# Kernel tuning notes

Hardware: AMD Instinct MI355X
Metric: run time of the kernel (lower is better)

The kernel has to match this reference:

```python
import jax, jax.numpy as jnp
import numpy as np

N = 20000      # nodes
E = 640000     # edges
H = 128        # hidden_channels
NB = 16        # num_angle_bins


def setup_inputs() -> dict:
    key = jax.random.key(0)
    ks = jax.random.split(key, 12)
    s = 0.05
    return {
        "x": jax.random.normal(ks[0], (N, H), jnp.float32),
        "pos": jax.random.normal(ks[1], (N, 3), jnp.float32),
        "edge_index": jax.random.randint(ks[2], (2, E), 0, N, dtype=jnp.int32).astype(jnp.int64),
        # edge_mlp: Linear(2H,H) -> silu -> Linear(H,H); weights stored [in,out]
        "W1": jax.random.normal(ks[3], (2 * H, H), jnp.float32) * s,
        "b1": jnp.zeros((H,), jnp.float32),
        "W2": jax.random.normal(ks[4], (H, H), jnp.float32) * s,
        "b2": jnp.zeros((H,), jnp.float32),
        "Wq": jax.random.normal(ks[5], (H, H), jnp.float32) * s,
        "bq": jnp.zeros((H,), jnp.float32),
        "Wk": jax.random.normal(ks[6], (H, H), jnp.float32) * s,
        "bk": jnp.zeros((H,), jnp.float32),
        "Wv": jax.random.normal(ks[7], (H, H), jnp.float32) * s,
        "bv": jnp.zeros((H,), jnp.float32),
    }


def reference(x, pos, edge_index, W1, b1, W2, b2, Wq, bq, Wk, bk, Wv, bv):
    num_nodes, hidden = x.shape
    num_bins = NB
    src = edge_index[0]  # node_i in torch code; PyG suffix _j gathers with this
    dst = edge_index[1]  # node_j in torch code; PyG suffix _i / aggregation index

    # per-edge embedding from endpoint node features  [E, H]
    h = jnp.concatenate([x[src], x[dst]], axis=-1)
    e = jax.nn.silu(h @ W1 + b1) @ W2 + b2

    # unit edge vectors  [E, 3]
    ev = pos[dst] - pos[src]
    ev = ev / (jnp.linalg.norm(ev, axis=1, keepdims=True) + 1e-8)

    q = e @ Wq + bq
    k = e @ Wk + bk
    v = e @ Wv + bv  # computed in torch forward but unused in message (kept for faithfulness)

    # PyG gathers these per-EDGE tensors by NODE indices (node_dim=0) -- replicate exactly
    e_j = e[src]           # [E, H]
    ev_i = ev[dst]         # [E, 3]
    ev_j = ev[src]         # [E, 3]
    q_i = q[dst]           # [E, H]
    k_j = k[src]           # [E, H]

    cos_theta = jnp.clip(jnp.sum(ev_i * ev_j, axis=-1), -1.0, 1.0)  # [E]
    angle_bins = jnp.linspace(-1.0, 1.0, num_bins + 1)
    bin_ids = jnp.clip(jnp.searchsorted(angle_bins, cos_theta, side="left") - 1, 0, num_bins - 1)

    attn_logits = jnp.sum(q_i * k_j, axis=-1) * (1.0 / np.sqrt(hidden))  # [E]

    # grouped softmax over (target_node, angle_bin) pairs, then weighted scatter-add
    group = dst * num_bins + bin_ids                     # [E]
    num_seg = num_nodes * num_bins
    m = jax.ops.segment_max(attn_logits, group, num_segments=num_seg)
    ex = jnp.exp(attn_logits - m[group])
    den = jax.ops.segment_sum(ex, group, num_segments=num_seg)
    attn = ex / (den[group] + 1e-16)                     # [E]

    summed = jax.ops.segment_sum(e_j * attn[:, None], group, num_segments=num_seg)  # [N*B, H]
    out = summed.reshape(num_nodes, num_bins, hidden)
    out = jnp.transpose(out, (0, 2, 1)).reshape(num_nodes, hidden * num_bins)  # [N, H*B]
    return out
```

## Files before the change

### kernel.cpp

```cpp
#include <hip/hip_runtime.h>

#define NN 20000
#define NE 640000
#define HH 128
#define NBIN 16
#define RSQRT_H 0.08838834764831845f

typedef short bf16x8 __attribute__((ext_vector_type(8)));
typedef float f32x4 __attribute__((ext_vector_type(4)));

__device__ __forceinline__ float b2f(unsigned short u) {
    return __uint_as_float(((unsigned)u) << 16);
}
__device__ __forceinline__ unsigned short f2b(float f) {
    unsigned u = __float_as_uint(f);
    unsigned r = (u + 0x7fffu + ((u >> 16) & 1u)) >> 16;
    return (unsigned short)r;
}
__device__ __forceinline__ int clampn(int v) {
    return min(max(v, 0), NN - 1);
}
__device__ __forceinline__ float dotdw(unsigned a, unsigned b) {
    float lo = __uint_as_float(a << 16) * __uint_as_float(b << 16);
    float hi = __uint_as_float(a & 0xffff0000u) * __uint_as_float(b & 0xffff0000u);
    return lo + hi;
}

__global__ void k_prep_w(const float* __restrict__ W1, const float* __restrict__ W2,
                         const float* __restrict__ Wq, const float* __restrict__ Wk,
                         ushort* __restrict__ W1T, ushort* __restrict__ W2T,
                         ushort* __restrict__ WqkT) {
    int i = blockIdx.x * 256 + threadIdx.x;
    if (i < 128 * 256) {
        int c = i >> 8, k = i & 255;
        W1T[i] = f2b(W1[k * 128 + c]);
    }
    if (i < 128 * 128) {
        int c = i >> 7, k = i & 127;
        W2T[i] = f2b(W2[k * 128 + c]);
    }
    if (i < 256 * 128) {
        int c = i >> 7, k = i & 127;
        float v = (c < 128) ? Wq[k * 128 + c] * RSQRT_H : Wk[k * 128 + (c - 128)];
        WqkT[i] = f2b(v);
    }
}

__global__ void k_prep_x(const float* __restrict__ x, ushort* __restrict__ xb) {
    int i = blockIdx.x * 256 + threadIdx.x;
    if (i >= NN * HH / 4) return;
    float4 v = ((const float4*)x)[i];
    ushort4 o;
    o.x = f2b(v.x); o.y = f2b(v.y); o.z = f2b(v.z); o.w = f2b(v.w);
    ((ushort4*)xb)[i] = o;
}

__global__ void k_ev(const int* __restrict__ ei, const float* __restrict__ pos,
                     float4* __restrict__ ev4) {
    int n = blockIdx.x * 256 + threadIdx.x;
    if (n >= NN) return;
    int s = clampn(ei[n]), d = clampn(ei[NE + n]);
    float dx = __fsub_rn(pos[d * 3 + 0], pos[s * 3 + 0]);
    float dy = __fsub_rn(pos[d * 3 + 1], pos[s * 3 + 1]);
    float dz = __fsub_rn(pos[d * 3 + 2], pos[s * 3 + 2]);
    float nsq = __fadd_rn(__fadd_rn(__fmul_rn(dx, dx), __fmul_rn(dy, dy)), __fmul_rn(dz, dz));
    float den = __fadd_rn(__fsqrt_rn(nsq), 1e-8f);
    float4 o;
    o.x = __fdiv_rn(dx, den); o.y = __fdiv_rn(dy, den); o.z = __fdiv_rn(dz, den); o.w = 0.f;
    ev4[n] = o;
}

__global__ __launch_bounds__(256) void k_mlp(
    const int* __restrict__ ei, const ushort* __restrict__ xb,
    const ushort* __restrict__ W1T, const ushort* __restrict__ W2T,
    const ushort* __restrict__ WqkT,
    const float* __restrict__ b1, const float* __restrict__ b2,
    const float* __restrict__ bq, const float* __restrict__ bk,
    ushort* __restrict__ ebuf, ushort* __restrict__ qbuf, ushort* __restrict__ kbuf)
{
    __shared__ ushort A[64][264];
    __shared__ ushort T[4][16][136];
    __shared__ ushort Eb[4][16][136];
    __shared__ int SN[64], DN[64];

    const int tid = threadIdx.x;
    const int wave = tid >> 6, lane = tid & 63;
    const int rw = lane & 15, kq = lane >> 4;
    const int m0 = blockIdx.x * 64;

    if (tid < 64)        SN[tid]      = (m0 + tid < NN)      ? clampn(ei[m0 + tid]) : 0;
    else if (tid < 128)  DN[tid - 64] = (m0 + tid - 64 < NN) ? clampn(ei[NE + m0 + tid - 64]) : 0;
    __syncthreads();

    const unsigned* x32 = (const unsigned*)xb;
    #pragma unroll
    for (int it = 0; it < 32; ++it) {
        int flat = tid + 256 * it;
        int r = flat >> 7, w = flat & 127;
        int node = (w < 64) ? SN[r] : DN[r];
        unsigned val = x32[node * 64 + (w & 63)];
        *(unsigned*)&A[r][2 * w] = val;
    }
    __syncthreads();

    f32x4 acc[8];
    #pragma unroll
    for (int c = 0; c < 8; c++) acc[c] = (f32x4){0.f, 0.f, 0.f, 0.f};
    for (int k0 = 0; k0 < 256; k0 += 32) {
        bf16x8 a = *(const bf16x8*)&A[wave * 16 + rw][k0 + 8 * kq];
        #pragma unroll
        for (int c = 0; c < 8; c++) {
            bf16x8 b = *(const bf16x8*)&W1T[(c * 16 + rw) * 256 + k0 + 8 * kq];
            acc[c] = __builtin_amdgcn_mfma_f32_16x16x32_bf16(a, b, acc[c], 0, 0, 0);
        }
    }
    #pragma unroll
    for (int c = 0; c < 8; c++) {
        float bias = b1[c * 16 + rw];
        #pragma unroll
        for (int r = 0; r < 4; r++) {
            float v = acc[c][r] + bias;
            float s = v / (1.f + __expf(-v));
            T[wave][kq * 4 + r][c * 16 + rw] = f2b(s);
        }
    }
    __syncthreads();

    f32x4 acc2[8];
    #pragma unroll
    for (int c = 0; c < 8; c++) acc2[c] = (f32x4){0.f, 0.f, 0.f, 0.f};
    for (int k0 = 0; k0 < 128; k0 += 32) {
        bf16x8 a = *(const bf16x8*)&T[wave][rw][k0 + 8 * kq];
        #pragma unroll
        for (int c = 0; c < 8; c++) {
            bf16x8 b = *(const bf16x8*)&W2T[(c * 16 + rw) * 128 + k0 + 8 * kq];
            acc2[c] = __builtin_amdgcn_mfma_f32_16x16x32_bf16(a, b, acc2[c], 0, 0, 0);
        }
    }
    #pragma unroll
    for (int c = 0; c < 8; c++) {
        float bias = b2[c * 16 + rw];
        #pragma unroll
        for (int r = 0; r < 4; r++) {
            float v = acc2[c][r] + bias;
            ushort hv = f2b(v);
            Eb[wave][kq * 4 + r][c * 16 + rw] = hv;
            int n = m0 + wave * 16 + kq * 4 + r;
            if (n < NN) ebuf[n * HH + c * 16 + rw] = hv;
        }
    }
    __syncthreads();

    f32x4 acc3[16];
    #pragma unroll
    for (int c = 0; c < 16; c++) acc3[c] = (f32x4){0.f, 0.f, 0.f, 0.f};
    for (int k0 = 0; k0 < 128; k0 += 32) {
        bf16x8 a = *(const bf16x8*)&Eb[wave][rw][k0 + 8 * kq];
        #pragma unroll
        for (int c = 0; c < 16; c++) {
            bf16x8 b = *(const bf16x8*)&WqkT[(c * 16 + rw) * 128 + k0 + 8 * kq];
            acc3[c] = __builtin_amdgcn_mfma_f32_16x16x32_bf16(a, b, acc3[c], 0, 0, 0);
        }
    }
    #pragma unroll
    for (int c = 0; c < 16; c++) {
        int col = c * 16 + rw;
        float bias = (col < 128) ? bq[col] * RSQRT_H : bk[col - 128];
        #pragma unroll
        for (int r = 0; r < 4; r++) {
            float v = acc3[c][r] + bias;
            int n = m0 + wave * 16 + kq * 4 + r;
            if (n < NN) {
                if (col < 128) qbuf[n * HH + col] = f2b(v);
                else           kbuf[n * HH + col - 128] = f2b(v);
            }
        }
    }
}

__global__ void k_hist(const int* __restrict__ ei, unsigned* __restrict__ cnt) {
    int e = blockIdx.x * 256 + threadIdx.x;
    if (e < NE) atomicAdd(&cnt[clampn(ei[NE + e])], 1u);
}

__global__ __launch_bounds__(1024) void k_scan(const unsigned* __restrict__ cnt,
                                               unsigned* __restrict__ starts,
                                               unsigned* __restrict__ cursor) {
    __shared__ unsigned vals[20480];
    __shared__ unsigned wsum[16];
    const int t = threadIdx.x;
    #pragma unroll
    for (int i = 0; i < 20; i++) {
        int idx = i * 1024 + t;
        vals[idx] = (idx < NN) ? cnt[idx] : 0u;
    }
    __syncthreads();
    const int base = t * 20;
    unsigned loc[20];
    unsigned s = 0;
    #pragma unroll
    for (int i = 0; i < 20; i++) { loc[i] = s; s += vals[base + i]; }
    const int lane = t & 63, wv = t >> 6;
    unsigned inc = s;
    #pragma unroll
    for (int o = 1; o < 64; o <<= 1) {
        unsigned y = __shfl_up(inc, o);
        if (lane >= o) inc += y;
    }
    if (lane == 63) wsum[wv] = inc;
    __syncthreads();
    unsigned wbase = 0;
    for (int i = 0; i < wv; i++) wbase += wsum[i];
    unsigned excl = wbase + inc - s;
    #pragma unroll
    for (int i = 0; i < 20; i++) {
        int idx = base + i;
        if (idx < NN) {
            unsigned val = excl + loc[i];
            starts[idx] = val;
            cursor[idx] = val;
        }
    }
    if (t == 1023) starts[NN] = wbase + inc;
}

__global__ __launch_bounds__(256) void k_edge(
    const int* __restrict__ ei, const ushort* __restrict__ qbuf,
    const ushort* __restrict__ kbuf, const float4* __restrict__ ev4,
    unsigned* __restrict__ cursor, uint2* __restrict__ sorted)
{
    int tid = blockIdx.x * 256 + threadIdx.x;
    int e = tid >> 2;
    int r = tid & 3;
    if (e >= NE) return;
    int s = clampn(ei[e]), d = clampn(ei[NE + e]);

    const uint4* q4 = (const uint4*)qbuf;
    const uint4* k4 = (const uint4*)kbuf;
    float p = 0.f;
    #pragma unroll
    for (int i = 0; i < 4; i++) {
        uint4 qw = q4[d * 16 + r * 4 + i];
        uint4 kw = k4[s * 16 + r * 4 + i];
        p += dotdw(qw.x, kw.x) + dotdw(qw.y, kw.y) + dotdw(qw.z, kw.z) + dotdw(qw.w, kw.w);
    }
    p += __shfl_xor(p, 1);
    p += __shfl_xor(p, 2);

    if (r == 0) {
        float4 vi = ev4[d], vj = ev4[s];
        float cosv = __fadd_rn(__fadd_rn(__fmul_rn(vi.x, vj.x), __fmul_rn(vi.y, vj.y)),
                               __fmul_rn(vi.z, vj.z));
        cosv = fminf(fmaxf(cosv, -1.f), 1.f);
        int cntb = 0;
        #pragma unroll
        for (int i = 0; i <= 16; i++) cntb += ((-1.f + 0.125f * (float)i) < cosv) ? 1 : 0;
        int b = min(max(cntb - 1, 0), NBIN - 1);
        unsigned pos = atomicAdd(&cursor[d], 1u);
        sorted[pos] = make_uint2(__float_as_uint(p), (unsigned)((s << 4) | b));
    }
}

__global__ __launch_bounds__(256) void k_node(
    const unsigned* __restrict__ starts, const uint2* __restrict__ sorted,
    const ushort* __restrict__ ebuf, float* __restrict__ out)
{
    const int wave = threadIdx.x >> 6, lane = threadIdx.x & 63;
    const int n = blockIdx.x * 4 + wave;
    __shared__ float tile[4][NBIN][132];
    __shared__ float den[4][NBIN];

    float* tw = &tile[wave][0][0];
    #pragma unroll
    for (int i = 0; i < 33; i++) {
        int idx = lane + 64 * i;
        if (idx < NBIN * 132) tw[idx] = 0.f;
    }
    if (lane < NBIN) den[wave][lane] = 0.f;

    const unsigned s0 = starts[n];
    const int deg = (int)(starts[n + 1] - s0);

    for (int j0 = 0; j0 < deg; j0 += 64) {
        int j = j0 + lane;
        if (j < deg) {
            uint2 m = sorted[s0 + j];
            atomicAdd(&den[wave][m.y & 15u], __expf(__uint_as_float(m.x)));
        }
    }
    if (lane < NBIN) den[wave][lane] = 1.f / (den[wave][lane] + 1e-16f);

    const unsigned* erow = (const unsigned*)ebuf;
    uint2 mN[4];
    #pragma unroll
    for (int i = 0; i < 4; i++)
        mN[i] = (i < deg) ? sorted[s0 + i] : make_uint2(0u, 0u);
    for (int jb = 0; jb < deg; jb += 4) {
        uint2 m[4];
        #pragma unroll
        for (int i = 0; i < 4; i++) m[i] = mN[i];
        #pragma unroll
        for (int i = 0; i < 4; i++) {
            int j = jb + 4 + i;
            mN[i] = (j < deg) ? sorted[s0 + j] : make_uint2(0u, 0u);
        }
        unsigned rv[4];
        #pragma unroll
        for (int i = 0; i < 4; i++)
            rv[i] = (jb + i < deg) ? erow[(m[i].y >> 4) * 64 + lane] : 0u;
        #pragma unroll
        for (int i = 0; i < 4; i++) {
            if (jb + i < deg) {
                int b = (int)(m[i].y & 15u);
                float w = __expf(__uint_as_float(m[i].x)) * den[wave][b];
                float2* p2 = (float2*)&tile[wave][b][2 * lane];
                float2 tv = *p2;
                tv.x += w * b2f((unsigned short)(rv[i] & 0xffffu));
                tv.y += w * b2f((unsigned short)(rv[i] >> 16));
                *p2 = tv;
            }
        }
    }

    #pragma unroll
    for (int i = 0; i < 8; i++) {
        int f4 = i * 64 + lane;
        int f0 = f4 * 4;
        int h = f0 >> 4, b0 = f0 & 15;
        float4 o;
        o.x = tile[wave][b0 + 0][h];
        o.y = tile[wave][b0 + 1][h];
        o.z = tile[wave][b0 + 2][h];
        o.w = tile[wave][b0 + 3][h];
        ((float4*)out)[(size_t)n * 512 + f4] = o;
    }
}

extern "C" void kernel_launch(void* const* d_in, const int* in_sizes, int n_in,
                              void* d_out, int out_size, void* d_ws, size_t ws_size,
                              hipStream_t stream) {
    const float* x        = (const float*)d_in[0];
    const float* pos      = (const float*)d_in[1];
    const int* ei         = (const int*)d_in[2];
    const float* W1       = (const float*)d_in[3];
    const float* b1       = (const float*)d_in[4];
    const float* W2       = (const float*)d_in[5];
    const float* b2       = (const float*)d_in[6];
    const float* Wq       = (const float*)d_in[7];
    const float* bq       = (const float*)d_in[8];
    const float* Wk       = (const float*)d_in[9];
    const float* bk       = (const float*)d_in[10];
    float* out = (float*)d_out;

    char* p = (char*)d_ws;
    auto take = [&](size_t bytes) -> char* {
        char* q = p;
        p += (bytes + 255) & ~(size_t)255;
        return q;
    };
    ushort* xb     = (ushort*)take((size_t)NN * HH * 2);
    ushort* ebuf   = (ushort*)take((size_t)NN * HH * 2);
    ushort* qbuf   = (ushort*)take((size_t)NN * HH * 2);
    ushort* kbuf   = (ushort*)take((size_t)NN * HH * 2);
    float4* ev4    = (float4*)take((size_t)NN * 16);
    ushort* W1T    = (ushort*)take(128 * 256 * 2);
    ushort* W2T    = (ushort*)take(128 * 128 * 2);
    ushort* WqkT   = (ushort*)take(256 * 128 * 2);
    unsigned* cnt  = (unsigned*)take((size_t)NN * 4);
    unsigned* starts = (unsigned*)take((size_t)(NN + 1) * 4);
    unsigned* cursor = (unsigned*)take((size_t)NN * 4);
    uint2* sorted  = (uint2*)take((size_t)NE * 8);
    if ((size_t)(p - (char*)d_ws) > ws_size) return;

    hipMemsetAsync(cnt, 0, (size_t)NN * 4, stream);
    k_prep_w<<<128, 256, 0, stream>>>(W1, W2, Wq, Wk, W1T, W2T, WqkT);
    k_prep_x<<<(NN * HH / 4 + 255) / 256, 256, 0, stream>>>(x, xb);
    k_ev<<<(NN + 255) / 256, 256, 0, stream>>>(ei, pos, ev4);
    k_mlp<<<(NN + 63) / 64, 256, 0, stream>>>(ei, xb, W1T, W2T, WqkT, b1, b2, bq, bk,
                                              ebuf, qbuf, kbuf);
    k_hist<<<(NE + 255) / 256, 256, 0, stream>>>(ei, cnt);
    k_scan<<<1, 1024, 0, stream>>>(cnt, starts, cursor);
    k_edge<<<(NE * 4 + 255) / 256, 256, 0, stream>>>(ei, qbuf, kbuf, ev4, cursor, sorted);
    k_node<<<NN / 4, 256, 0, stream>>>(starts, sorted, ebuf, out);
}
```

Baseline: 408.2 us.

## Merge prep kernels and memset into one launch; accumulate node bins in registers

```diff
diff --git a/kernel.cpp b/kernel.cpp
--- a/kernel.cpp
+++ b/kernel.cpp
@@ -26,48 +26,55 @@
     return lo + hi;
 }
 
-__global__ void k_prep_w(const float* __restrict__ W1, const float* __restrict__ W2,
-                         const float* __restrict__ Wq, const float* __restrict__ Wk,
-                         ushort* __restrict__ W1T, ushort* __restrict__ W2T,
-                         ushort* __restrict__ WqkT) {
-    int i = blockIdx.x * 256 + threadIdx.x;
-    if (i < 128 * 256) {
-        int c = i >> 8, k = i & 255;
-        W1T[i] = f2b(W1[k * 128 + c]);
-    }
-    if (i < 128 * 128) {
-        int c = i >> 7, k = i & 127;
-        W2T[i] = f2b(W2[k * 128 + c]);
-    }
-    if (i < 256 * 128) {
-        int c = i >> 7, k = i & 127;
-        float v = (c < 128) ? Wq[k * 128 + c] * RSQRT_H : Wk[k * 128 + (c - 128)];
-        WqkT[i] = f2b(v);
-    }
-}
-
-__global__ void k_prep_x(const float* __restrict__ x, ushort* __restrict__ xb) {
-    int i = blockIdx.x * 256 + threadIdx.x;
-    if (i >= NN * HH / 4) return;
-    float4 v = ((const float4*)x)[i];
-    ushort4 o;
-    o.x = f2b(v.x); o.y = f2b(v.y); o.z = f2b(v.z); o.w = f2b(v.w);
-    ((ushort4*)xb)[i] = o;
-}
-
-__global__ void k_ev(const int* __restrict__ ei, const float* __restrict__ pos,
-                     float4* __restrict__ ev4) {
-    int n = blockIdx.x * 256 + threadIdx.x;
-    if (n >= NN) return;
-    int s = clampn(ei[n]), d = clampn(ei[NE + n]);
-    float dx = __fsub_rn(pos[d * 3 + 0], pos[s * 3 + 0]);
-    float dy = __fsub_rn(pos[d * 3 + 1], pos[s * 3 + 1]);
-    float dz = __fsub_rn(pos[d * 3 + 2], pos[s * 3 + 2]);
-    float nsq = __fadd_rn(__fadd_rn(__fmul_rn(dx, dx), __fmul_rn(dy, dy)), __fmul_rn(dz, dz));
-    float den = __fadd_rn(__fsqrt_rn(nsq), 1e-8f);
-    float4 o;
-    o.x = __fdiv_rn(dx, den); o.y = __fdiv_rn(dy, den); o.z = __fdiv_rn(dz, den); o.w = 0.f;
-    ev4[n] = o;
+__global__ __launch_bounds__(256) void k_prep(
+    const float* __restrict__ x, ushort* __restrict__ xb,
+    const int* __restrict__ ei, const float* __restrict__ pos, float4* __restrict__ ev4,
+    const float* __restrict__ W1, const float* __restrict__ W2,
+    const float* __restrict__ Wq, const float* __restrict__ Wk,
+    ushort* __restrict__ W1T, ushort* __restrict__ W2T, ushort* __restrict__ WqkT,
+    unsigned* __restrict__ cnt)
+{
+    const int bid = blockIdx.x, tid = threadIdx.x;
+    if (bid < 2500) {
+        int i = bid * 256 + tid;
+        float4 v = ((const float4*)x)[i];
+        ushort4 o;
+        o.x = f2b(v.x); o.y = f2b(v.y); o.z = f2b(v.z); o.w = f2b(v.w);
+        ((ushort4*)xb)[i] = o;
+    } else if (bid < 2579) {
+        int n = (bid - 2500) * 256 + tid;
+        if (n < NN) {
+            int s = clampn(ei[n]), d = clampn(ei[NE + n]);
+            float dx = __fsub_rn(pos[d * 3 + 0], pos[s * 3 + 0]);
+            float dy = __fsub_rn(pos[d * 3 + 1], pos[s * 3 + 1]);
+            float dz = __fsub_rn(pos[d * 3 + 2], pos[s * 3 + 2]);
+            float nsq = __fadd_rn(__fadd_rn(__fmul_rn(dx, dx), __fmul_rn(dy, dy)),
+                                  __fmul_rn(dz, dz));
+            float den = __fadd_rn(__fsqrt_rn(nsq), 1e-8f);
+            float4 o;
+            o.x = __fdiv_rn(dx, den); o.y = __fdiv_rn(dy, den);
+            o.z = __fdiv_rn(dz, den); o.w = 0.f;
+            ev4[n] = o;
+        }
+    } else if (bid < 2707) {
+        int i = (bid - 2579) * 256 + tid;
+        if (i < 128 * 256) {
+            int c = i >> 8, k = i & 255;
+            W1T[i] = f2b(W1[k * 128 + c]);
+        }
+        if (i < 128 * 128) {
+            int c = i >> 7, k = i & 127;
+            W2T[i] = f2b(W2[k * 128 + c]);
+        }
+        if (i < 256 * 128) {
+            int c = i >> 7, k = i & 127;
+            float v = (c < 128) ? Wq[k * 128 + c] * RSQRT_H : Wk[k * 128 + (c - 128)];
+            WqkT[i] = f2b(v);
+        }
+    } else {
+        int i = (bid - 2707) * 256 + tid;
+        if (i < NN) cnt[i] = 0u;
+    }
 }
 
 __global__ __launch_bounds__(256) void k_mlp(
@@ -267,17 +274,9 @@
 {
     const int wave = threadIdx.x >> 6, lane = threadIdx.x & 63;
     const int n = blockIdx.x * 4 + wave;
-    __shared__ float tile[4][NBIN][132];
     __shared__ float den[4][NBIN];
 
-    float* tw = &tile[wave][0][0];
-    #pragma unroll
-    for (int i = 0; i < 33; i++) {
-        int idx = lane + 64 * i;
-        if (idx < NBIN * 132) tw[idx] = 0.f;
-    }
     if (lane < NBIN) den[wave][lane] = 0.f;
-
     const unsigned s0 = starts[n];
     const int deg = (int)(starts[n + 1] - s0);
 
@@ -290,11 +289,17 @@
     }
     if (lane < NBIN) den[wave][lane] = 1.f / (den[wave][lane] + 1e-16f);
 
+    float accx[NBIN], accy[NBIN];
+    #pragma unroll
+    for (int i = 0; i < NBIN; i++) { accx[i] = 0.f; accy[i] = 0.f; }
+
     const unsigned* erow = (const unsigned*)ebuf;
     uint2 mN[4];
     #pragma unroll
     for (int i = 0; i < 4; i++)
         mN[i] = (i < deg) ? sorted[s0 + i] : make_uint2(0u, 0u);
+
+#define ACC_CASE(K) case K: accx[K] += w * vx; accy[K] += w * vy; break;
     for (int jb = 0; jb < deg; jb += 4) {
         uint2 m[4];
         #pragma unroll
@@ -311,28 +316,36 @@
         #pragma unroll
         for (int i = 0; i < 4; i++) {
             if (jb + i < deg) {
-                int b = (int)(m[i].y & 15u);
+                int b = (int)__builtin_amdgcn_readfirstlane(m[i].y & 15u);
                 float w = __expf(__uint_as_float(m[i].x)) * den[wave][b];
-                float2* p2 = (float2*)&tile[wave][b][2 * lane];
-                float2 tv = *p2;
-                tv.x += w * b2f((unsigned short)(rv[i] & 0xffffu));
-                tv.y += w * b2f((unsigned short)(rv[i] >> 16));
-                *p2 = tv;
+                float vx = w, vy = w;
+                vx = b2f((unsigned short)(rv[i] & 0xffffu));
+                vy = b2f((unsigned short)(rv[i] >> 16));
+                switch (b) {
+                    ACC_CASE(0) ACC_CASE(1) ACC_CASE(2) ACC_CASE(3)
+                    ACC_CASE(4) ACC_CASE(5) ACC_CASE(6) ACC_CASE(7)
+                    ACC_CASE(8) ACC_CASE(9) ACC_CASE(10) ACC_CASE(11)
+                    ACC_CASE(12) ACC_CASE(13) ACC_CASE(14) ACC_CASE(15)
+                }
             }
         }
     }
-
-    #pragma unroll
-    for (int i = 0; i < 8; i++) {
-        int f4 = i * 64 + lane;
-        int f0 = f4 * 4;
-        int h = f0 >> 4, b0 = f0 & 15;
+#undef ACC_CASE
+
+    float* op = out + (size_t)n * (HH * NBIN) + 32 * lane;
+    #pragma unroll
+    for (int j = 0; j < 4; j++) {
         float4 o;
-        o.x = tile[wave][b0 + 0][h];
-        o.y = tile[wave][b0 + 1][h];
-        o.z = tile[wave][b0 + 2][h];
-        o.w = tile[wave][b0 + 3][h];
-        ((float4*)out)[(size_t)n * 512 + f4] = o;
+        o.x = accx[4 * j + 0]; o.y = accx[4 * j + 1];
+        o.z = accx[4 * j + 2]; o.w = accx[4 * j + 3];
+        ((float4*)op)[j] = o;
+    }
+    #pragma unroll
+    for (int j = 0; j < 4; j++) {
+        float4 o;
+        o.x = accy[4 * j + 0]; o.y = accy[4 * j + 1];
+        o.z = accy[4 * j + 2]; o.w = accy[4 * j + 3];
+        ((float4*)op)[4 + j] = o;
     }
 }
 
@@ -372,10 +385,8 @@
     uint2* sorted  = (uint2*)take((size_t)NE * 8);
     if ((size_t)(p - (char*)d_ws) > ws_size) return;
 
-    hipMemsetAsync(cnt, 0, (size_t)NN * 4, stream);
-    k_prep_w<<<128, 256, 0, stream>>>(W1, W2, Wq, Wk, W1T, W2T, WqkT);
-    k_prep_x<<<(NN * HH / 4 + 255) / 256, 256, 0, stream>>>(x, xb);
-    k_ev<<<(NN + 255) / 256, 256, 0, stream>>>(ei, pos, ev4);
+    k_prep<<<2786, 256, 0, stream>>>(x, xb, ei, pos, ev4, W1, W2, Wq, Wk,
+                                     W1T, W2T, WqkT, cnt);
     k_mlp<<<(NN + 63) / 64, 256, 0, stream>>>(ei, xb, W1T, W2T, WqkT, b1, b2, bq, bk,
                                               ebuf, qbuf, kbuf);
     k_hist<<<(NE + 255) / 256, 256, 0, stream>>>(ei, cnt);
```

Result: slower. 430.5 us (+5.5%).
